# Kernel optimization log

Measured on AMD Instinct MI355X. Metric: run time of the kernel, lower is better.

Reference implementation:

```python
import jax, jax.numpy as jnp
import numpy as np

N_NODES = 50000
N_EDGES = 1600000
NFEAT, NHID, NCLASS = 512, 128, 40


def setup_inputs() -> dict:
    key = jax.random.key(0)
    ks = jax.random.split(key, 10)
    x = jax.random.normal(ks[0], (N_NODES, NFEAT), dtype=jnp.float32)
    edge_src = jax.random.randint(ks[1], (N_EDGES,), 0, N_NODES, dtype=jnp.int32)
    edge_dst = jax.random.randint(ks[2], (N_EDGES,), 0, N_NODES, dtype=jnp.int32)
    edge_weight = jax.random.uniform(ks[3], (N_EDGES,), dtype=jnp.float32)
    # GraphConvolution params: gc1 (nfeat->nhid), one additional (nhid->nhid), gc2 (nhid->nclass)
    s1 = 1.0 / np.sqrt(NHID)
    s2 = 1.0 / np.sqrt(NCLASS)
    W1 = jax.random.uniform(ks[4], (NFEAT, NHID), minval=-s1, maxval=s1, dtype=jnp.float32)
    b1 = jax.random.uniform(ks[5], (NHID,), minval=-s1, maxval=s1, dtype=jnp.float32)
    Wh = jax.random.uniform(ks[6], (NHID, NHID), minval=-s1, maxval=s1, dtype=jnp.float32)
    bh = jax.random.uniform(ks[7], (NHID,), minval=-s1, maxval=s1, dtype=jnp.float32)
    W2 = jax.random.uniform(ks[8], (NHID, NCLASS), minval=-s2, maxval=s2, dtype=jnp.float32)
    b2 = jax.random.uniform(ks[9], (NCLASS,), minval=-s2, maxval=s2, dtype=jnp.float32)
    return {"x": x, "edge_src": edge_src, "edge_dst": edge_dst, "edge_weight": edge_weight,
            "W1": W1, "b1": b1, "Wh": Wh, "bh": bh, "W2": W2, "b2": b2}


def reference(x, edge_src, edge_dst, edge_weight, W1, b1, Wh, bh, W2, b2):
    def spmm(h):
        # out[i] = sum_j adj[i, j] * h[j]  with adj given as weighted edge list (src=j, dst=i)
        return jax.ops.segment_sum(edge_weight[:, None] * h[edge_src], edge_dst,
                                   num_segments=x.shape[0])

    def gconv(h, W, b):
        return spmm(h @ W) + b  # dense transform then sparse aggregation

    h = jax.nn.relu(gconv(x, W1, b1))       # gc1
    h = jax.nn.relu(gconv(h, Wh, bh))        # additional hidden layer
    h = gconv(h, W2, b2)                     # gc2
    return jax.nn.log_softmax(h, axis=1)
```

## Files before the change

kernel.cpp:

```cpp
#include <hip/hip_runtime.h>
#include <hip/hip_bf16.h>
#include <hip/hip_fp8.h>
#include <math.h>

#define N_NODES 50000
#define N_EDGES 1600000
#define NFEAT 512
#define NHID 128
#define NCLASS 40

#define NBUCKETS 196
#define BUCKET_CAP 16384

typedef __attribute__((ext_vector_type(8))) short bf16x8;
typedef __attribute__((ext_vector_type(4))) float f32x4;
typedef __attribute__((ext_vector_type(2))) float f32x2;

static __device__ __forceinline__ float asfloat_u32(unsigned int u) {
    union { unsigned int u; float f; } c;
    c.u = u;
    return c.f;
}
static __device__ __forceinline__ unsigned int asu32_f(float f) {
    union { float f; unsigned int u; } c;
    c.f = f;
    return c.u;
}
static __device__ __forceinline__ unsigned short f2bf(float f) {
    union { float f; unsigned int u; } c;
    c.f = f;
    unsigned int r = c.u + 0x7FFFu + ((c.u >> 16) & 1u);
    return (unsigned short)(r >> 16);
}

static __device__ __forceinline__ float fp8_to_f32_sw(unsigned int x) {
    float m = asfloat_u32((x & 0x7Fu) << 20) * 0x1p+120f;
    return asfloat_u32(asu32_f(m) | ((x & 0x80u) << 24));
}
static __device__ __forceinline__ void dq4(unsigned int u, float* f) {
#if __has_builtin(__builtin_amdgcn_cvt_pk_f32_fp8)
    f32x2 lo = __builtin_amdgcn_cvt_pk_f32_fp8(u, false);
    f32x2 hi = __builtin_amdgcn_cvt_pk_f32_fp8(u, true);
    f[0] = lo[0]; f[1] = lo[1]; f[2] = hi[0]; f[3] = hi[1];
#else
    f[0] = fp8_to_f32_sw(u & 0xFFu);
    f[1] = fp8_to_f32_sw((u >> 8) & 0xFFu);
    f[2] = fp8_to_f32_sw((u >> 16) & 0xFFu);
    f[3] = fp8_to_f32_sw((u >> 24) & 0xFFu);
#endif
}
static __device__ __forceinline__ unsigned char f2fp8(float f) {
#if __has_builtin(__builtin_amdgcn_cvt_pk_fp8_f32)
    int v = __builtin_amdgcn_cvt_pk_fp8_f32(f, f, 0, false);
    return (unsigned char)(v & 0xFF);
#else
    __hip_fp8_e4m3 h(f);
    return (unsigned char)h.__x;
#endif
}

__global__ __launch_bounds__(256) void prep_kernel(const float* __restrict__ W1,
                                                   unsigned short* __restrict__ Wt1,
                                                   const float* __restrict__ Wh,
                                                   unsigned short* __restrict__ Wth,
                                                   const float* __restrict__ W2,
                                                   unsigned short* __restrict__ Wt2,
                                                   int* __restrict__ bucketCursor) {
    int idx = blockIdx.x * 256 + threadIdx.x;
    if (idx < NFEAT * NHID) {
        int k = idx >> 7;
        int n = idx & 127;
        Wt1[(size_t)n * NFEAT + k] = f2bf(W1[idx]);
    } else if (idx < NFEAT * NHID + NHID * NHID) {
        int j = idx - NFEAT * NHID;
        int k = j >> 7;
        int n = j & 127;
        Wth[(size_t)n * NHID + k] = f2bf(Wh[j]);
    } else if (idx < NFEAT * NHID + NHID * NHID + 64 * NHID) {
        int j = idx - (NFEAT * NHID + NHID * NHID);
        int n = j & 63;
        int k = j >> 6;
        Wt2[(size_t)n * NHID + k] = (n < NCLASS) ? f2bf(W2[(size_t)k * NCLASS + n]) : 0;
    } else {
        int j = idx - (NFEAT * NHID + NHID * NHID + 64 * NHID);
        if (j < NBUCKETS) bucketCursor[j] = j * BUCKET_CAP;
    }
}

#define LDPB 72
#define GEMM_LDS_BYTES (128 * LDPB * 2)

template <bool A_IS_BF16, bool OUT_FP8>
static __device__ __forceinline__ void gemm64_body(const void* __restrict__ Ap,
                                                   const unsigned short* __restrict__ Wt,
                                                   void* __restrict__ Cv,
                                                   const int M, const int K,
                                                   char* smem, int bid) {
    unsigned short* Bs = (unsigned short*)smem;
    const int tid = threadIdx.x;
    const int wave = tid >> 6;
    const int lane = tid & 63;
    const int ln = lane & 15;
    const int quad = lane >> 4;
    const int row0 = bid * 64;

    const int arow = row0 + wave * 16 + ln;
    const bool aOk = arow < M;
    const unsigned short* Abf = (const unsigned short*)Ap + (size_t)arow * K + quad * 8;
    const float* Af = (const float*)Ap + (size_t)arow * K + quad * 8;

    const int bn = tid >> 1;
    const int bk = (tid & 1) * 32;
    const unsigned short* Bg = Wt + (size_t)bn * K + bk;

    f32x4 acc[8];
#pragma unroll
    for (int t = 0; t < 8; ++t) acc[t] = (f32x4){0.f, 0.f, 0.f, 0.f};

    for (int kc = 0; kc < K; kc += 64) {
        bf16x8 qb0 = *(const bf16x8*)(Bg + kc);
        bf16x8 qb1 = *(const bf16x8*)(Bg + kc + 8);
        bf16x8 qb2 = *(const bf16x8*)(Bg + kc + 16);
        bf16x8 qb3 = *(const bf16x8*)(Bg + kc + 24);

        bf16x8 a0, a1;
        if (A_IS_BF16) {
            if (aOk) {
                a0 = *(const bf16x8*)(Abf + kc);
                a1 = *(const bf16x8*)(Abf + kc + 32);
            } else {
#pragma unroll
                for (int j = 0; j < 8; ++j) { a0[j] = 0; a1[j] = 0; }
            }
        } else {
            if (aOk) {
                float4 f0 = *(const float4*)(Af + kc);
                float4 f1 = *(const float4*)(Af + kc + 4);
                float4 f2 = *(const float4*)(Af + kc + 32);
                float4 f3 = *(const float4*)(Af + kc + 36);
                a0[0] = (short)f2bf(f0.x); a0[1] = (short)f2bf(f0.y);
                a0[2] = (short)f2bf(f0.z); a0[3] = (short)f2bf(f0.w);
                a0[4] = (short)f2bf(f1.x); a0[5] = (short)f2bf(f1.y);
                a0[6] = (short)f2bf(f1.z); a0[7] = (short)f2bf(f1.w);
                a1[0] = (short)f2bf(f2.x); a1[1] = (short)f2bf(f2.y);
                a1[2] = (short)f2bf(f2.z); a1[3] = (short)f2bf(f2.w);
                a1[4] = (short)f2bf(f3.x); a1[5] = (short)f2bf(f3.y);
                a1[6] = (short)f2bf(f3.z); a1[7] = (short)f2bf(f3.w);
            } else {
#pragma unroll
                for (int j = 0; j < 8; ++j) { a0[j] = 0; a1[j] = 0; }
            }
        }

        __syncthreads();
        *(bf16x8*)&Bs[bn * LDPB + bk] = qb0;
        *(bf16x8*)&Bs[bn * LDPB + bk + 8] = qb1;
        *(bf16x8*)&Bs[bn * LDPB + bk + 16] = qb2;
        *(bf16x8*)&Bs[bn * LDPB + bk + 24] = qb3;
        __syncthreads();

#pragma unroll
        for (int t = 0; t < 8; ++t) {
            bf16x8 b0 = *(const bf16x8*)&Bs[(t * 16 + ln) * LDPB + quad * 8];
            acc[t] = __builtin_amdgcn_mfma_f32_16x16x32_bf16(a0, b0, acc[t], 0, 0, 0);
        }
#pragma unroll
        for (int t = 0; t < 8; ++t) {
            bf16x8 b1 = *(const bf16x8*)&Bs[(t * 16 + ln) * LDPB + 32 + quad * 8];
            acc[t] = __builtin_amdgcn_mfma_f32_16x16x32_bf16(a1, b1, acc[t], 0, 0, 0);
        }
    }

    if (OUT_FP8) {
        unsigned char* C8 = (unsigned char*)Cv;
#pragma unroll
        for (int t = 0; t < 8; ++t) {
#pragma unroll
            for (int r = 0; r < 4; ++r) {
                int row = row0 + wave * 16 + quad * 4 + r;
                if (row < M) C8[(size_t)row * 128 + t * 16 + ln] = f2fp8(acc[t][r]);
            }
        }
    } else {
        unsigned short* C = (unsigned short*)Cv;
#pragma unroll
        for (int t = 0; t < 8; ++t) {
#pragma unroll
            for (int r = 0; r < 4; ++r) {
                int row = row0 + wave * 16 + quad * 4 + r;
                if (row < M) C[(size_t)row * 128 + t * 16 + ln] = f2bf(acc[t][r]);
            }
        }
    }
}

static __device__ __forceinline__ void bin_body(const int* __restrict__ src,
                                                const int* __restrict__ dst,
                                                const float* __restrict__ w,
                                                int* __restrict__ bucketCursor,
                                                uint2* __restrict__ binned,
                                                int n, char* smem, int bid) {
    int* hist = (int*)smem;
    int* cur = (int*)smem + NBUCKETS;
    const int tid = threadIdx.x;
    const int base = bid * 4096;
    if (tid < NBUCKETS) hist[tid] = 0;
    __syncthreads();
#pragma unroll
    for (int r = 0; r < 16; ++r) {
        int e = base + r * 256 + tid;
        if (e < n) atomicAdd(&hist[dst[e] >> 8], 1);
    }
    __syncthreads();
    if (tid < NBUCKETS && hist[tid] > 0)
        cur[tid] = atomicAdd(&bucketCursor[tid], hist[tid]);
    __syncthreads();
#pragma unroll
    for (int r = 0; r < 16; ++r) {
        int e = base + r * 256 + tid;
        if (e < n) {
            int d = dst[e];
            int pos = atomicAdd(&cur[d >> 8], 1);
            uint2 rec;
            rec.x = (unsigned int)src[e] | ((unsigned int)(d & 255) << 16);
            rec.y = asu32_f(w[e]);
            binned[pos] = rec;
        }
    }
}

#define GEMM1_BLOCKS 782
#define BIN_BLOCKS 391
__global__ __launch_bounds__(256) void fused_gemm1_bin(const float* __restrict__ x,
                                                       const unsigned short* __restrict__ Wt1,
                                                       unsigned char* __restrict__ tb,
                                                       const int* __restrict__ src,
                                                       const int* __restrict__ dst,
                                                       const float* __restrict__ w,
                                                       int* __restrict__ bucketCursor,
                                                       uint2* __restrict__ binned) {
    __shared__ char smem[GEMM_LDS_BYTES];
    if (blockIdx.x < GEMM1_BLOCKS) {
        gemm64_body<false, true>(x, Wt1, tb, N_NODES, NFEAT, smem, blockIdx.x);
    } else {
        bin_body(src, dst, w, bucketCursor, binned, N_EDGES, smem,
                 blockIdx.x - GEMM1_BLOCKS);
    }
}

#define LDP2 136
__global__ __launch_bounds__(256) void gemm64_l2(const unsigned short* __restrict__ A,
                                                 const unsigned short* __restrict__ Wt,
                                                 unsigned char* __restrict__ C) {
    __shared__ unsigned short Bs[128 * LDP2];
    const int tid = threadIdx.x;
    const int wave = tid >> 6;
    const int lane = tid & 63;
    const int ln = lane & 15;
    const int quad = lane >> 4;
    const int row0 = blockIdx.x * 64;
    const int arow = row0 + wave * 16 + ln;
    const bool aOk = arow < N_NODES;
    const unsigned short* Abf = A + (size_t)arow * 128 + quad * 8;

    bf16x8 a0, a1, a2, a3;
    if (aOk) {
        a0 = *(const bf16x8*)(Abf);
        a1 = *(const bf16x8*)(Abf + 32);
        a2 = *(const bf16x8*)(Abf + 64);
        a3 = *(const bf16x8*)(Abf + 96);
    } else {
#pragma unroll
        for (int j = 0; j < 8; ++j) { a0[j] = 0; a1[j] = 0; a2[j] = 0; a3[j] = 0; }
    }

#pragma unroll
    for (int i = 0; i < 8; ++i) {
        int q = tid + 256 * i;
        int r = q >> 4;
        int c = (q & 15) * 8;
        *(bf16x8*)&Bs[r * LDP2 + c] = *(const bf16x8*)(Wt + (size_t)r * 128 + c);
    }
    __syncthreads();

    f32x4 acc[8];
#pragma unroll
    for (int t = 0; t < 8; ++t) acc[t] = (f32x4){0.f, 0.f, 0.f, 0.f};

#pragma unroll
    for (int t = 0; t < 8; ++t) {
        bf16x8 b = *(const bf16x8*)&Bs[(t * 16 + ln) * LDP2 + quad * 8];
        acc[t] = __builtin_amdgcn_mfma_f32_16x16x32_bf16(a0, b, acc[t], 0, 0, 0);
    }
#pragma unroll
    for (int t = 0; t < 8; ++t) {
        bf16x8 b = *(const bf16x8*)&Bs[(t * 16 + ln) * LDP2 + 32 + quad * 8];
        acc[t] = __builtin_amdgcn_mfma_f32_16x16x32_bf16(a1, b, acc[t], 0, 0, 0);
    }
#pragma unroll
    for (int t = 0; t < 8; ++t) {
        bf16x8 b = *(const bf16x8*)&Bs[(t * 16 + ln) * LDP2 + 64 + quad * 8];
        acc[t] = __builtin_amdgcn_mfma_f32_16x16x32_bf16(a2, b, acc[t], 0, 0, 0);
    }
#pragma unroll
    for (int t = 0; t < 8; ++t) {
        bf16x8 b = *(const bf16x8*)&Bs[(t * 16 + ln) * LDP2 + 96 + quad * 8];
        acc[t] = __builtin_amdgcn_mfma_f32_16x16x32_bf16(a3, b, acc[t], 0, 0, 0);
    }

#pragma unroll
    for (int t = 0; t < 8; ++t) {
#pragma unroll
        for (int r = 0; r < 4; ++r) {
            int row = row0 + wave * 16 + quad * 4 + r;
            if (row < N_NODES) C[(size_t)row * 128 + t * 16 + ln] = f2fp8(acc[t][r]);
        }
    }
}

__global__ __launch_bounds__(1024) void build_csr(const uint2* __restrict__ binned,
                                                  const int* __restrict__ bucketCursor,
                                                  unsigned int* __restrict__ pairs,
                                                  int* __restrict__ row_ptr) {
    __shared__ int bs[256];
    __shared__ int hist[256];
    __shared__ int sc[256];
    __shared__ int cur[256];
    const int b = blockIdx.x;
    const int tid = threadIdx.x;

    if (tid < 256) bs[tid] = (tid < NBUCKETS) ? (bucketCursor[tid] - tid * BUCKET_CAP) : 0;
    if (tid < 256) hist[tid] = 0;
    __syncthreads();
    for (int off = 1; off < 256; off <<= 1) {
        int t = 0;
        if (tid < 256 && tid >= off) t = bs[tid - off];
        __syncthreads();
        if (tid < 256) bs[tid] += t;
        __syncthreads();
    }
    const int cnt = bucketCursor[b] - b * BUCKET_CAP;
    const int segStart = bs[b] - cnt;
    if (b == NBUCKETS - 1 && tid == 0) row_ptr[N_NODES] = bs[NBUCKETS - 1];
    const uint2* seg = binned + (size_t)b * BUCKET_CAP;

    for (int i = tid; i < cnt; i += 1024)
        atomicAdd(&hist[seg[i].x >> 16], 1);
    __syncthreads();
    if (tid < 256) {
        int v = hist[tid];
        sc[tid] = v;
    }
    __syncthreads();
    for (int off = 1; off < 256; off <<= 1) {
        int t = 0;
        if (tid < 256 && tid >= off) t = sc[tid - off];
        __syncthreads();
        if (tid < 256) sc[tid] += t;
        __syncthreads();
    }
    if (tid < 256) {
        int excl = sc[tid] - hist[tid];
        int node = b * 256 + tid;
        if (node < N_NODES) row_ptr[node] = segStart + excl;
        cur[tid] = segStart + excl;
    }
    __syncthreads();
    for (int i = tid; i < cnt; i += 1024) {
        uint2 p = seg[i];
        int pos = atomicAdd(&cur[p.x >> 16], 1);
        pairs[pos] = (p.x & 0xFFFFu) | ((unsigned int)f2bf(asfloat_u32(p.y)) << 16);
    }
}

__global__ __launch_bounds__(256) void gemm_n64(const unsigned short* __restrict__ A,
                                                const unsigned short* __restrict__ Wt2,
                                                unsigned char* __restrict__ C, int M) {
    __shared__ unsigned short As[64 * LDP2];
    __shared__ unsigned short Bs2[64 * LDP2];
    const int tid = threadIdx.x;
    const int wave = tid >> 6;
    const int lane = tid & 63;
    const int ln = lane & 15;
    const int quad = lane >> 4;
    const int row0 = blockIdx.x * 64;

#pragma unroll
    for (int i = 0; i < 4; ++i) {
        int q = tid + 256 * i;
        int r = q >> 4;
        int c = (q & 15) * 8;
        bf16x8 v;
        if (row0 + r < M) {
            v = *(const bf16x8*)(A + (size_t)(row0 + r) * 128 + c);
        } else {
#pragma unroll
            for (int j = 0; j < 8; ++j) v[j] = 0;
        }
        *(bf16x8*)&As[r * LDP2 + c] = v;
    }
#pragma unroll
    for (int i = 0; i < 4; ++i) {
        int q = tid + 256 * i;
        int r = q >> 4;
        int c = (q & 15) * 8;
        *(bf16x8*)&Bs2[r * LDP2 + c] = *(const bf16x8*)(Wt2 + (size_t)r * 128 + c);
    }
    __syncthreads();

    f32x4 acc[4];
#pragma unroll
    for (int t = 0; t < 4; ++t) acc[t] = (f32x4){0.f, 0.f, 0.f, 0.f};

#pragma unroll
    for (int kc = 0; kc < 128; kc += 32) {
        bf16x8 a = *(const bf16x8*)&As[(wave * 16 + ln) * LDP2 + kc + quad * 8];
#pragma unroll
        for (int t = 0; t < 4; ++t) {
            bf16x8 b = *(const bf16x8*)&Bs2[(t * 16 + ln) * LDP2 + kc + quad * 8];
            acc[t] = __builtin_amdgcn_mfma_f32_16x16x32_bf16(a, b, acc[t], 0, 0, 0);
        }
    }

#pragma unroll
    for (int t = 0; t < 4; ++t) {
#pragma unroll
        for (int r = 0; r < 4; ++r) {
            int row = row0 + wave * 16 + quad * 4 + r;
            if (row < M) C[(size_t)row * 64 + t * 16 + ln] = f2fp8(acc[t][r]);
        }
    }
}

__global__ __launch_bounds__(256) void spmm_bias_relu_fp8(const unsigned char* __restrict__ t,
                                                          const int* __restrict__ row_ptr,
                                                          const unsigned int* __restrict__ pairs,
                                                          const float* __restrict__ bias,
                                                          unsigned short* __restrict__ out) {
    const int node = blockIdx.x * 4 + (threadIdx.x >> 6);
    const int lane = threadIdx.x & 63;
    const int g = lane >> 4;
    const int fl = (lane & 15) * 8;
    const int e0 = row_ptr[node];
    const int e1 = row_ptr[node + 1];
    float acc8[8];
#pragma unroll
    for (int j = 0; j < 8; ++j) acc8[j] = 0.f;

    int e = e0;
    for (; e + 32 <= e1; e += 32) {
        unsigned int p[8];
        uint2 v[8];
#pragma unroll
        for (int i = 0; i < 8; ++i) p[i] = pairs[e + 4 * i + g];
#pragma unroll
        for (int i = 0; i < 8; ++i)
            v[i] = *(const uint2*)(t + (size_t)(p[i] & 0xFFFFu) * 128 + fl);
#pragma unroll
        for (int i = 0; i < 8; ++i) {
            float w = asfloat_u32(p[i] & 0xFFFF0000u);
            float f[8];
            dq4(v[i].x, f);
            dq4(v[i].y, f + 4);
#pragma unroll
            for (int j = 0; j < 8; ++j) acc8[j] += w * f[j];
        }
    }
    for (; e + 4 <= e1; e += 4) {
        unsigned int p = pairs[e + g];
        uint2 v = *(const uint2*)(t + (size_t)(p & 0xFFFFu) * 128 + fl);
        float w = asfloat_u32(p & 0xFFFF0000u);
        float f[8];
        dq4(v.x, f);
        dq4(v.y, f + 4);
#pragma unroll
        for (int j = 0; j < 8; ++j) acc8[j] += w * f[j];
    }
    if (g < e1 - e) {
        unsigned int p = pairs[e + g];
        uint2 v = *(const uint2*)(t + (size_t)(p & 0xFFFFu) * 128 + fl);
        float w = asfloat_u32(p & 0xFFFF0000u);
        float f[8];
        dq4(v.x, f);
        dq4(v.y, f + 4);
#pragma unroll
        for (int j = 0; j < 8; ++j) acc8[j] += w * f[j];
    }
#pragma unroll
    for (int j = 0; j < 8; ++j) {
        acc8[j] += __shfl_xor(acc8[j], 16);
        acc8[j] += __shfl_xor(acc8[j], 32);
    }
    if (g == 0) {
        float4 b0 = *(const float4*)&bias[fl];
        float4 b1 = *(const float4*)&bias[fl + 4];
        acc8[0] = fmaxf(acc8[0] + b0.x, 0.f);
        acc8[1] = fmaxf(acc8[1] + b0.y, 0.f);
        acc8[2] = fmaxf(acc8[2] + b0.z, 0.f);
        acc8[3] = fmaxf(acc8[3] + b0.w, 0.f);
        acc8[4] = fmaxf(acc8[4] + b1.x, 0.f);
        acc8[5] = fmaxf(acc8[5] + b1.y, 0.f);
        acc8[6] = fmaxf(acc8[6] + b1.z, 0.f);
        acc8[7] = fmaxf(acc8[7] + b1.w, 0.f);
        uint4 o;
        o.x = ((unsigned int)f2bf(acc8[0])) | (((unsigned int)f2bf(acc8[1])) << 16);
        o.y = ((unsigned int)f2bf(acc8[2])) | (((unsigned int)f2bf(acc8[3])) << 16);
        o.z = ((unsigned int)f2bf(acc8[4])) | (((unsigned int)f2bf(acc8[5])) << 16);
        o.w = ((unsigned int)f2bf(acc8[6])) | (((unsigned int)f2bf(acc8[7])) << 16);
        *(uint4*)(out + (size_t)node * 128 + fl) = o;
    }
}

__global__ __launch_bounds__(256) void spmm_logsoftmax(const unsigned char* __restrict__ t,
                                                       const int* __restrict__ row_ptr,
                                                       const unsigned int* __restrict__ pairs,
                                                       const float* __restrict__ bias,
                                                       float* __restrict__ out) {
    const int node = blockIdx.x * 4 + (threadIdx.x >> 6);
    const int lane = threadIdx.x & 63;
    const int g = lane >> 4;
    const int fe = (lane & 15) * 4;
    const int e0 = row_ptr[node];
    const int e1 = row_ptr[node + 1];
    float a0 = 0.f, a1 = 0.f, a2 = 0.f, a3 = 0.f;
    int e = e0;
    for (; e + 32 <= e1; e += 32) {
        unsigned int p[8];
        unsigned int v[8];
#pragma unroll
        for (int i = 0; i < 8; ++i) p[i] = pairs[e + 4 * i + g];
#pragma unroll
        for (int i = 0; i < 8; ++i)
            v[i] = *(const unsigned int*)(t + (size_t)(p[i] & 0xFFFFu) * 64 + fe);
#pragma unroll
        for (int i = 0; i < 8; ++i) {
            float w = asfloat_u32(p[i] & 0xFFFF0000u);
            float f[4];
            dq4(v[i], f);
            a0 += w * f[0];
            a1 += w * f[1];
            a2 += w * f[2];
            a3 += w * f[3];
        }
    }
    for (; e + 4 <= e1; e += 4) {
        unsigned int p = pairs[e + g];
        unsigned int v = *(const unsigned int*)(t + (size_t)(p & 0xFFFFu) * 64 + fe);
        float w = asfloat_u32(p & 0xFFFF0000u);
        float f[4];
        dq4(v, f);
        a0 += w * f[0]; a1 += w * f[1]; a2 += w * f[2]; a3 += w * f[3];
    }
    if (g < e1 - e) {
        unsigned int p = pairs[e + g];
        unsigned int v = *(const unsigned int*)(t + (size_t)(p & 0xFFFFu) * 64 + fe);
        float w = asfloat_u32(p & 0xFFFF0000u);
        float f[4];
        dq4(v, f);
        a0 += w * f[0]; a1 += w * f[1]; a2 += w * f[2]; a3 += w * f[3];
    }
    a0 += __shfl_xor(a0, 16); a0 += __shfl_xor(a0, 32);
    a1 += __shfl_xor(a1, 16); a1 += __shfl_xor(a1, 32);
    a2 += __shfl_xor(a2, 16); a2 += __shfl_xor(a2, 32);
    a3 += __shfl_xor(a3, 16); a3 += __shfl_xor(a3, 32);

    const bool valid = (lane & 15) < 10;
    float l0 = -INFINITY, l1 = -INFINITY, l2 = -INFINITY, l3 = -INFINITY;
    if (valid) {
        float4 b = *(const float4*)&bias[fe];
        l0 = a0 + b.x; l1 = a1 + b.y; l2 = a2 + b.z; l3 = a3 + b.w;
    }
    float m = fmaxf(fmaxf(l0, l1), fmaxf(l2, l3));
#pragma unroll
    for (int off = 8; off; off >>= 1) m = fmaxf(m, __shfl_xor(m, off));
    float s = valid ? (__expf(l0 - m) + __expf(l1 - m) + __expf(l2 - m) + __expf(l3 - m)) : 0.f;
#pragma unroll
    for (int off = 8; off; off >>= 1) s += __shfl_xor(s, off);
    if (valid && g == 0) {
        float ls = __logf(s);
        float4 o;
        o.x = l0 - m - ls; o.y = l1 - m - ls; o.z = l2 - m - ls; o.w = l3 - m - ls;
        *(float4*)&out[(size_t)node * NCLASS + fe] = o;
    }
}


extern "C" void kernel_launch(void* const* d_in, const int* in_sizes, int n_in,
                              void* d_out, int out_size, void* d_ws, size_t ws_size,
                              hipStream_t stream) {
    const float* x = (const float*)d_in[0];
    const int* edge_src = (const int*)d_in[1];
    const int* edge_dst = (const int*)d_in[2];
    const float* edge_weight = (const float*)d_in[3];
    const float* W1 = (const float*)d_in[4];
    const float* b1 = (const float*)d_in[5];
    const float* Wh = (const float*)d_in[6];
    const float* bh = (const float*)d_in[7];
    const float* W2 = (const float*)d_in[8];
    const float* b2 = (const float*)d_in[9];
    float* out = (float*)d_out;

    size_t off = 0;
    auto carve = [&](size_t bytes) {
        void* p = (char*)d_ws + off;
        off += (bytes + 511) & ~(size_t)511;
        return p;
    };
    unsigned char* tb = (unsigned char*)carve((size_t)N_NODES * 128);
    unsigned short* hb = (unsigned short*)carve((size_t)N_NODES * 128 * 2);
    unsigned char* t3 = (unsigned char*)carve((size_t)N_NODES * 64);
    unsigned short* Wt1 = (unsigned short*)carve((size_t)NFEAT * NHID * 2);
    unsigned short* Wth = (unsigned short*)carve((size_t)NHID * NHID * 2);
    unsigned short* Wt2 = (unsigned short*)carve((size_t)64 * NHID * 2);
    int* row_ptr = (int*)carve((size_t)(N_NODES + 4) * 4);
    int* bucketCursor = (int*)carve((size_t)NBUCKETS * 4);
    uint2* binned = (uint2*)carve((size_t)NBUCKETS * BUCKET_CAP * 8);
    unsigned int* pairs = (unsigned int*)carve((size_t)N_EDGES * 4);
    (void)ws_size; (void)n_in; (void)in_sizes; (void)out_size;

    const int prepBlocks =
        (NFEAT * NHID + NHID * NHID + 64 * NHID + NBUCKETS + 255) / 256;
    const int spmmBlocks = N_NODES / 4;
    const int gemmBlocks = (N_NODES + 63) / 64;

    prep_kernel<<<prepBlocks, 256, 0, stream>>>(W1, Wt1, Wh, Wth, W2, Wt2, bucketCursor);

    fused_gemm1_bin<<<GEMM1_BLOCKS + BIN_BLOCKS, 256, 0, stream>>>(
        x, Wt1, tb, edge_src, edge_dst, edge_weight, bucketCursor, binned);

    build_csr<<<NBUCKETS, 1024, 0, stream>>>(binned, bucketCursor, pairs, row_ptr);

    spmm_bias_relu_fp8<<<spmmBlocks, 256, 0, stream>>>(tb, row_ptr, pairs, b1, hb);

    gemm64_l2<<<gemmBlocks, 256, 0, stream>>>(hb, Wth, tb);
    spmm_bias_relu_fp8<<<spmmBlocks, 256, 0, stream>>>(tb, row_ptr, pairs, bh, hb);

    gemm_n64<<<gemmBlocks, 256, 0, stream>>>(hb, Wt2, t3, N_NODES);
    spmm_logsoftmax<<<spmmBlocks, 256, 0, stream>>>(t3, row_ptr, pairs, b2, out);
}
```

Baseline: 355.9 us.

## Split fp8 hidden features into two 64-column planes for SpMM gather

The fp8 GEMM outputs for layers 1 and 2 are now written as two separate planes of 64 columns each, instead of one 128-byte row per node. The hidden-layer SpMM makes two passes, one per plane, with 8 lanes per edge and 8 edges in flight per wave. This is meant to shrink the gathered working set per pass so each half-table (about 3.2 MB) fits better in cache. The cost is that the pairs and row_ptr are read twice, there is an extra shuffle reduction step, and the GEMM epilogue issues more scattered byte stores.

```diff
diff --git a/kernel.cpp b/kernel.cpp
--- a/kernel.cpp
+++ b/kernel.cpp
@@ -11,6 +11,8 @@
 
 #define NBUCKETS 196
 #define BUCKET_CAP 16384
+
+#define PLANE ((size_t)N_NODES * 64)
 
 typedef __attribute__((ext_vector_type(8))) short bf16x8;
 typedef __attribute__((ext_vector_type(4))) float f32x4;
@@ -90,10 +92,10 @@
 #define LDPB 72
 #define GEMM_LDS_BYTES (128 * LDPB * 2)
 
-template <bool A_IS_BF16, bool OUT_FP8>
+template <bool A_IS_BF16>
 static __device__ __forceinline__ void gemm64_body(const void* __restrict__ Ap,
                                                    const unsigned short* __restrict__ Wt,
-                                                   void* __restrict__ Cv,
+                                                   unsigned char* __restrict__ C8,
                                                    const int M, const int K,
                                                    char* smem, int bid) {
     unsigned short* Bs = (unsigned short*)smem;
@@ -171,25 +173,14 @@
         }
     }
 
-    if (OUT_FP8) {
-        unsigned char* C8 = (unsigned char*)Cv;
-#pragma unroll
-        for (int t = 0; t < 8; ++t) {
-#pragma unroll
-            for (int r = 0; r < 4; ++r) {
-                int row = row0 + wave * 16 + quad * 4 + r;
-                if (row < M) C8[(size_t)row * 128 + t * 16 + ln] = f2fp8(acc[t][r]);
-            }
-        }
-    } else {
-        unsigned short* C = (unsigned short*)Cv;
-#pragma unroll
-        for (int t = 0; t < 8; ++t) {
-#pragma unroll
-            for (int r = 0; r < 4; ++r) {
-                int row = row0 + wave * 16 + quad * 4 + r;
-                if (row < M) C[(size_t)row * 128 + t * 16 + ln] = f2bf(acc[t][r]);
-            }
+#pragma unroll
+    for (int t = 0; t < 8; ++t) {
+        int col = t * 16 + ln;
+        unsigned char* Cp = C8 + (size_t)(col >> 6) * PLANE + (col & 63);
+#pragma unroll
+        for (int r = 0; r < 4; ++r) {
+            int row = row0 + wave * 16 + quad * 4 + r;
+            if (row < M) Cp[(size_t)row * 64] = f2fp8(acc[t][r]);
         }
     }
 }
@@ -241,7 +232,7 @@
                                                        uint2* __restrict__ binned) {
     __shared__ char smem[GEMM_LDS_BYTES];
     if (blockIdx.x < GEMM1_BLOCKS) {
-        gemm64_body<false, true>(x, Wt1, tb, N_NODES, NFEAT, smem, blockIdx.x);
+        gemm64_body<false>(x, Wt1, tb, N_NODES, NFEAT, smem, blockIdx.x);
     } else {
         bin_body(src, dst, w, bucketCursor, binned, N_EDGES, smem,
                  blockIdx.x - GEMM1_BLOCKS);
@@ -310,10 +301,12 @@
 
 #pragma unroll
     for (int t = 0; t < 8; ++t) {
+        int col = t * 16 + ln;
+        unsigned char* Cp = C + (size_t)(col >> 6) * PLANE + (col & 63);
 #pragma unroll
         for (int r = 0; r < 4; ++r) {
             int row = row0 + wave * 16 + quad * 4 + r;
-            if (row < N_NODES) C[(size_t)row * 128 + t * 16 + ln] = f2fp8(acc[t][r]);
+            if (row < N_NODES) Cp[(size_t)row * 64] = f2fp8(acc[t][r]);
         }
     }
 }
@@ -439,75 +432,82 @@
                                                           unsigned short* __restrict__ out) {
     const int node = blockIdx.x * 4 + (threadIdx.x >> 6);
     const int lane = threadIdx.x & 63;
-    const int g = lane >> 4;
-    const int fl = (lane & 15) * 8;
+    const int g = lane >> 3;
+    const int fl = (lane & 7) * 8;
     const int e0 = row_ptr[node];
     const int e1 = row_ptr[node + 1];
-    float acc8[8];
-#pragma unroll
-    for (int j = 0; j < 8; ++j) acc8[j] = 0.f;
-
-    int e = e0;
-    for (; e + 32 <= e1; e += 32) {
-        unsigned int p[8];
-        uint2 v[8];
-#pragma unroll
-        for (int i = 0; i < 8; ++i) p[i] = pairs[e + 4 * i + g];
-#pragma unroll
-        for (int i = 0; i < 8; ++i)
-            v[i] = *(const uint2*)(t + (size_t)(p[i] & 0xFFFFu) * 128 + fl);
-#pragma unroll
-        for (int i = 0; i < 8; ++i) {
-            float w = asfloat_u32(p[i] & 0xFFFF0000u);
+
+#pragma unroll
+    for (int h = 0; h < 2; ++h) {
+        const unsigned char* tbl = t + (size_t)h * PLANE;
+        float acc8[8];
+#pragma unroll
+        for (int j = 0; j < 8; ++j) acc8[j] = 0.f;
+
+        int e = e0;
+        for (; e + 32 <= e1; e += 32) {
+            unsigned int p[4];
+            uint2 v[4];
+#pragma unroll
+            for (int i = 0; i < 4; ++i) p[i] = pairs[e + 8 * i + g];
+#pragma unroll
+            for (int i = 0; i < 4; ++i)
+                v[i] = *(const uint2*)(tbl + (size_t)(p[i] & 0xFFFFu) * 64 + fl);
+#pragma unroll
+            for (int i = 0; i < 4; ++i) {
+                float w = asfloat_u32(p[i] & 0xFFFF0000u);
+                float f[8];
+                dq4(v[i].x, f);
+                dq4(v[i].y, f + 4);
+#pragma unroll
+                for (int j = 0; j < 8; ++j) acc8[j] += w * f[j];
+            }
+        }
+        for (; e + 8 <= e1; e += 8) {
+            unsigned int p = pairs[e + g];
+            uint2 v = *(const uint2*)(tbl + (size_t)(p & 0xFFFFu) * 64 + fl);
+            float w = asfloat_u32(p & 0xFFFF0000u);
             float f[8];
-            dq4(v[i].x, f);
-            dq4(v[i].y, f + 4);
+            dq4(v.x, f);
+            dq4(v.y, f + 4);
 #pragma unroll
             for (int j = 0; j < 8; ++j) acc8[j] += w * f[j];
         }
-    }
-    for (; e + 4 <= e1; e += 4) {
-        unsigned int p = pairs[e + g];
-        uint2 v = *(const uint2*)(t + (size_t)(p & 0xFFFFu) * 128 + fl);
-        float w = asfloat_u32(p & 0xFFFF0000u);
-        float f[8];
-        dq4(v.x, f);
-        dq4(v.y, f + 4);
-#pragma unroll
-        for (int j = 0; j < 8; ++j) acc8[j] += w * f[j];
-    }
-    if (g < e1 - e) {
-        unsigned int p = pairs[e + g];
-        uint2 v = *(const uint2*)(t + (size_t)(p & 0xFFFFu) * 128 + fl);
-        float w = asfloat_u32(p & 0xFFFF0000u);
-        float f[8];
-        dq4(v.x, f);
-        dq4(v.y, f + 4);
-#pragma unroll
-        for (int j = 0; j < 8; ++j) acc8[j] += w * f[j];
-    }
-#pragma unroll
-    for (int j = 0; j < 8; ++j) {
-        acc8[j] += __shfl_xor(acc8[j], 16);
-        acc8[j] += __shfl_xor(acc8[j], 32);
-    }
-    if (g == 0) {
-        float4 b0 = *(const float4*)&bias[fl];
-        float4 b1 = *(const float4*)&bias[fl + 4];
-        acc8[0] = fmaxf(acc8[0] + b0.x, 0.f);
-        acc8[1] = fmaxf(acc8[1] + b0.y, 0.f);
-        acc8[2] = fmaxf(acc8[2] + b0.z, 0.f);
-        acc8[3] = fmaxf(acc8[3] + b0.w, 0.f);
-        acc8[4] = fmaxf(acc8[4] + b1.x, 0.f);
-        acc8[5] = fmaxf(acc8[5] + b1.y, 0.f);
-        acc8[6] = fmaxf(acc8[6] + b1.z, 0.f);
-        acc8[7] = fmaxf(acc8[7] + b1.w, 0.f);
-        uint4 o;
-        o.x = ((unsigned int)f2bf(acc8[0])) | (((unsigned int)f2bf(acc8[1])) << 16);
-        o.y = ((unsigned int)f2bf(acc8[2])) | (((unsigned int)f2bf(acc8[3])) << 16);
-        o.z = ((unsigned int)f2bf(acc8[4])) | (((unsigned int)f2bf(acc8[5])) << 16);
-        o.w = ((unsigned int)f2bf(acc8[6])) | (((unsigned int)f2bf(acc8[7])) << 16);
-        *(uint4*)(out + (size_t)node * 128 + fl) = o;
+        if (g < e1 - e) {
+            unsigned int p = pairs[e + g];
+            uint2 v = *(const uint2*)(tbl + (size_t)(p & 0xFFFFu) * 64 + fl);
+            float w = asfloat_u32(p & 0xFFFF0000u);
+            float f[8];
+            dq4(v.x, f);
+            dq4(v.y, f + 4);
+#pragma unroll
+            for (int j = 0; j < 8; ++j) acc8[j] += w * f[j];
+        }
+#pragma unroll
+        for (int j = 0; j < 8; ++j) {
+            acc8[j] += __shfl_xor(acc8[j], 8);
+            acc8[j] += __shfl_xor(acc8[j], 16);
+            acc8[j] += __shfl_xor(acc8[j], 32);
+        }
+        if (g == 0) {
+            const int fb = h * 64 + fl;
+            float4 b0 = *(const float4*)&bias[fb];
+            float4 b1 = *(const float4*)&bias[fb + 4];
+            acc8[0] = fmaxf(acc8[0] + b0.x, 0.f);
+            acc8[1] = fmaxf(acc8[1] + b0.y, 0.f);
+            acc8[2] = fmaxf(acc8[2] + b0.z, 0.f);
+            acc8[3] = fmaxf(acc8[3] + b0.w, 0.f);
+            acc8[4] = fmaxf(acc8[4] + b1.x, 0.f);
+            acc8[5] = fmaxf(acc8[5] + b1.y, 0.f);
+            acc8[6] = fmaxf(acc8[6] + b1.z, 0.f);
+            acc8[7] = fmaxf(acc8[7] + b1.w, 0.f);
+            uint4 o;
+            o.x = ((unsigned int)f2bf(acc8[0])) | (((unsigned int)f2bf(acc8[1])) << 16);
+            o.y = ((unsigned int)f2bf(acc8[2])) | (((unsigned int)f2bf(acc8[3])) << 16);
+            o.z = ((unsigned int)f2bf(acc8[4])) | (((unsigned int)f2bf(acc8[5])) << 16);
+            o.w = ((unsigned int)f2bf(acc8[6])) | (((unsigned int)f2bf(acc8[7])) << 16);
+            *(uint4*)(out + (size_t)node * 128 + fb) = o;
+        }
     }
 }
 
```

Measured after the change: 375.9 us. 1.06x slower.
